# Performance work log

Hardware: AMD Instinct MI355X
Metric: run time of the kernel (lower is better)

The kernel has to match this reference:

```python
import jax, jax.numpy as jnp
import numpy as np

N = 10000      # total_num (hardcoded in GraphLearning)
BS = 100       # batch_size for per-chunk BatchNorm in training mode
C = 128        # out_channels (feature dim)
K = 50         # topk
NHID = 256     # ngcn_layers
NCLASS = 10
GAMMA = 0.01   # gamma_reg
EPS = 1e-5     # BatchNorm eps


def setup_inputs() -> dict:
    key = jax.random.key(0)
    ks = jax.random.split(key, 6)
    return {
        "inputs": jax.random.normal(ks[0], (N, 3, 32, 32), jnp.float32),
        "W_lin": jax.random.normal(ks[1], (3 * 32 * 32, C), jnp.float32) * 0.02,
        "b_lin": jnp.zeros((C,), jnp.float32),
        "bn_gamma": jnp.ones((C,), jnp.float32),
        "bn_beta": jnp.zeros((C,), jnp.float32),
        "a_S": jax.random.normal(ks[2], (C,), jnp.float32) * 0.1,
        "b_S": jnp.zeros((1,), jnp.float32),
        "W1": jax.random.normal(ks[3], (C, NHID), jnp.float32) * 0.05,
        "b1": jnp.zeros((NHID,), jnp.float32),
        "W2": jax.random.normal(ks[4], (NHID, NCLASS), jnp.float32) * 0.05,
        "b2": jnp.zeros((NCLASS,), jnp.float32),
    }


def reference(inputs, W_lin, b_lin, bn_gamma, bn_beta, a_S, b_S, W1, b1, W2, b2):
    # --- GraphLearning.forward: chunked linear + per-chunk BatchNorm (training mode) ---
    flat = inputs.reshape(N, -1)                      # [N, 3072]
    out = flat @ W_lin + b_lin                        # [N, C]
    ch = out.reshape(N // BS, BS, C)                  # per-100-row chunks, each BN'd with its own stats
    mu = ch.mean(axis=1, keepdims=True)
    var = ch.var(axis=1, keepdims=True)               # biased var, as torch BN uses
    feat = (((ch - mu) * jax.lax.rsqrt(var + EPS)).reshape(N, C)) * bn_gamma + bn_beta

    # --- construct_graph_S_loop, vectorized ---
    # per-row score: relu(a^T (x_i - x_j)^2 + b) = relu(p_i + p_j - 2 x_i diag(a) x_j^T + b)
    p = (feat ** 2) @ a_S                             # [N]
    G = (feat * a_S) @ feat.T                         # [N, N]
    scores = jax.nn.relu(p[:, None] + p[None, :] - 2.0 * G + b_S[0])
    vals, idx = jax.lax.top_k(scores, K)              # [N, K]
    soft = jax.nn.softmax(vals, axis=-1)              # softmax over each row's top-k scores
    S = jnp.zeros((N, N), feat.dtype).at[jnp.arange(N)[:, None], idx].set(soft)

    # --- loss_GL = sum(pairwise_dist * S) + gamma * sum(S); S nonzero only at (i, idx[i]) ---
    xn = (feat ** 2).sum(axis=1)                      # [N]
    nb = feat[idx]                                    # [N, K, C]
    dp = jnp.clip(xn[:, None] + xn[idx] - 2.0 * jnp.einsum('nc,nkc->nk', feat, nb), 0.0)
    loss_GL = (dp * soft).sum() + GAMMA * soft.sum()

    # --- GCN (eval mode: dropout off) ---
    h = jax.nn.relu(S @ (feat @ W1) + b1)             # gc1 + relu
    logits = S @ (h @ W2) + b2                        # gc2
    semi = jax.nn.log_softmax(logits, axis=1)
    return semi, loss_GL, S
```

## Files before the change

### kernel.cpp

```cpp
#include <hip/hip_runtime.h>
#include <hip/hip_bf16.h>
#include <cstdint>
#include <cstddef>

#define N_TOT 10000
#define CDIM  128
#define TK    50
#define NHID_ 256
#define NCLS  10
#define GAMMA_REG 0.01f
#define BN_EPS 1e-5f

typedef float f32x4 __attribute__((ext_vector_type(4)));
typedef short s16x8 __attribute__((ext_vector_type(8)));

__device__ __forceinline__ float waveSumF(float v){
  #pragma unroll
  for (int o=32;o;o>>=1) v += __shfl_xor(v,o,64);
  return v;
}
__device__ __forceinline__ float waveMaxF(float v){
  #pragma unroll
  for (int o=32;o;o>>=1) v = fmaxf(v,__shfl_xor(v,o,64));
  return v;
}
__device__ __forceinline__ int waveSumI(int v){
  #pragma unroll
  for (int o=32;o;o>>=1) v += __shfl_xor(v,o,64);
  return v;
}
__device__ __forceinline__ ushort bfh(float f){
  __hip_bfloat16 h = __float2bfloat16(f);
  return *reinterpret_cast<ushort*>(&h);
}
__device__ __forceinline__ float bf2f(ushort u){
  __hip_bfloat16 h = *reinterpret_cast<__hip_bfloat16*>(&u);
  return __bfloat162float(h);
}
__device__ __forceinline__ void gload16(const void* g, void* l){
  __builtin_amdgcn_global_load_lds(
      (const __attribute__((address_space(1))) void*)g,
      (__attribute__((address_space(3))) void*)l, 16, 0, 0);
}

template<bool BIAS>
__global__ __launch_bounds__(256) void gemm64(const float* __restrict__ A,
                                              const float* __restrict__ B,
                                              const float* __restrict__ bias,
                                              float* __restrict__ C,
                                              int M, int N, int K){
  constexpr int BK=32;
  __shared__ float As[BK][64+4];
  __shared__ float Bs[BK][64+4];
  const int tid = threadIdx.x;
  const int bm = blockIdx.y*64, bn = blockIdx.x*64;
  const int tm = (tid>>4)<<2;
  const int tn = (tid&15)<<2;
  float acc[4][4] = {};
  for (int k0=0;k0<K;k0+=BK){
    #pragma unroll
    for (int i=0;i<2;++i){
      int fi = tid + i*256;
      int r  = fi>>3;
      int c4 = fi&7;
      float4 v = make_float4(0,0,0,0);
      int gr = bm + r;
      if (gr < M) v = *(const float4*)(A + (size_t)gr*K + k0 + (c4<<2));
      As[(c4<<2)+0][r]=v.x; As[(c4<<2)+1][r]=v.y; As[(c4<<2)+2][r]=v.z; As[(c4<<2)+3][r]=v.w;
    }
    #pragma unroll
    for (int i=0;i<2;++i){
      int fi = tid + i*256;
      int r  = fi>>4;
      int c4 = fi&15;
      float4 v = *(const float4*)(B + (size_t)(k0+r)*N + bn + (c4<<2));
      *(float4*)&Bs[r][c4<<2] = v;
    }
    __syncthreads();
    #pragma unroll
    for (int kk=0;kk<BK;++kk){
      float a[4], b[4];
      *(float4*)a = *(const float4*)&As[kk][tm];
      *(float4*)b = *(const float4*)&Bs[kk][tn];
      #pragma unroll
      for (int i=0;i<4;++i)
        #pragma unroll
        for (int j=0;j<4;++j) acc[i][j] = fmaf(a[i], b[j], acc[i][j]);
    }
    __syncthreads();
  }
  #pragma unroll
  for (int i=0;i<4;++i){
    int gr = bm+tm+i;
    if (gr < M){
      float4 o; o.x=acc[i][0]; o.y=acc[i][1]; o.z=acc[i][2]; o.w=acc[i][3];
      if (BIAS){
        o.x += bias[bn+tn+0]; o.y += bias[bn+tn+1];
        o.z += bias[bn+tn+2]; o.w += bias[bn+tn+3];
      }
      *(float4*)(C + (size_t)gr*N + bn + tn) = o;
    }
  }
}

__global__ __launch_bounds__(256) void wtprep(const float* __restrict__ W,
                                              ushort* __restrict__ Wth,
                                              ushort* __restrict__ Wtl){
  __shared__ float t[64][129];
  const int tid = threadIdx.x;
  const int kb = blockIdx.x*64;
  #pragma unroll
  for (int it=0; it<8; ++it){
    int cs = it*256 + tid;
    int kr = cs >> 5;
    int c4 = cs & 31;
    float4 v = *(const float4*)(W + (size_t)(kb+kr)*128 + c4*4);
    t[kr][c4*4+0]=v.x; t[kr][c4*4+1]=v.y; t[kr][c4*4+2]=v.z; t[kr][c4*4+3]=v.w;
  }
  __syncthreads();
  #pragma unroll
  for (int it=0; it<4; ++it){
    int ch = it*256 + tid;
    int n  = ch >> 3;
    int k8 = (ch & 7)*8;
    s16x8 hv, lv;
    #pragma unroll
    for (int e=0;e<8;++e){
      float v = t[k8+e][n];
      ushort h = bfh(v);
      hv[e] = (short)h;
      lv[e] = (short)bfh(v - bf2f(h));
    }
    *(s16x8*)(Wth + (size_t)n*3072 + kb + k8) = hv;
    *(s16x8*)(Wtl + (size_t)n*3072 + kb + k8) = lv;
  }
}

__global__ __launch_bounds__(256,2) void lin_mfma(const float* __restrict__ Ain,
                                                  const ushort* __restrict__ Wth,
                                                  const ushort* __restrict__ Wtl,
                                                  float* __restrict__ P){
  extern __shared__ char lds[];
  ushort* ldsu = (ushort*)lds;
  const int tid = threadIdx.x, lane = tid&63, wave = tid>>6;
  const int wm = wave>>1, wn = wave&1;
  const int mt = blockIdx.x % 79, kc = blockIdx.x / 79;
  const int bm = mt*128;
  const int lr = lane&15, kq = lane>>4;
  f32x4 acc[4][4] = {};

  for (int st=0; st<6; ++st){
    const int kb = kc*384 + st*64;
    if (st) __syncthreads();
    #pragma unroll
    for (int it=0; it<8; ++it){
      int cs = it*256+tid, row = cs>>4, c4 = cs&15;
      int rg = bm+row; rg = rg < N_TOT ? rg : N_TOT-1;
      float4 v = *(const float4*)(Ain + (size_t)rg*3072 + kb + c4*4);
      ushort4 h, l;
      h.x=bfh(v.x); l.x=bfh(v.x-bf2f(h.x));
      h.y=bfh(v.y); l.y=bfh(v.y-bf2f(h.y));
      h.z=bfh(v.z); l.z=bfh(v.z-bf2f(h.z));
      h.w=bfh(v.w); l.w=bfh(v.w-bf2f(h.w));
      int bo = (c4*8) ^ ((row&7)<<4);
      *(ushort4*)(lds + row*128 + bo)         = h;
      *(ushort4*)(lds + 16384 + row*128 + bo) = l;
    }
    #pragma unroll
    for (int it=0; it<4; ++it){
      int cs = it*256+tid, row = cs>>3, slot = cs&7;
      int srcb = (slot*16) ^ ((row&7)<<4);
      gload16(Wth + (size_t)row*3072 + kb + (srcb>>1), ldsu + 16384 + cs*8);
      gload16(Wtl + (size_t)row*3072 + kb + (srcb>>1), ldsu + 24576 + cs*8);
    }
    __syncthreads();
    #pragma unroll
    for (int ks=0; ks<2; ++ks){
      const int kbyte = ks*64 + kq*16;
      s16x8 yh[4], yl[4];
      #pragma unroll
      for (int j=0;j<4;++j){
        int ma = wm*64 + j*16 + lr;
        int oa = ma*128 + (kbyte ^ ((ma&7)<<4));
        yh[j] = *(const s16x8*)(lds + oa);
        yl[j] = *(const s16x8*)(lds + 16384 + oa);
      }
      #pragma unroll
      for (int i=0;i<4;++i){
        int na = wn*64 + i*16 + lr;
        int ob = na*128 + (kbyte ^ ((na&7)<<4));
        s16x8 xh = *(const s16x8*)(lds + 32768 + ob);
        s16x8 xl = *(const s16x8*)(lds + 49152 + ob);
        #pragma unroll
        for (int j=0;j<4;++j){
          acc[i][j] = __builtin_amdgcn_mfma_f32_16x16x32_bf16(xh, yh[j], acc[i][j],0,0,0);
          acc[i][j] = __builtin_amdgcn_mfma_f32_16x16x32_bf16(xh, yl[j], acc[i][j],0,0,0);
          acc[i][j] = __builtin_amdgcn_mfma_f32_16x16x32_bf16(xl, yh[j], acc[i][j],0,0,0);
        }
      }
    }
  }
  #pragma unroll
  for (int j=0;j<4;++j){
    int m = bm + wm*64 + j*16 + lr;
    if (m < N_TOT){
      float* Pr = P + ((size_t)kc*N_TOT + m)*CDIM;
      #pragma unroll
      for (int i=0;i<4;++i)
        *(f32x4*)(Pr + wn*64 + i*16 + kq*4) = acc[i][j];
    }
  }
}

__global__ __launch_bounds__(256) void lin_reduce(const float* __restrict__ P,
                                                  const float* __restrict__ bias,
                                                  float* __restrict__ feat){
  int e = blockIdx.x*256 + threadIdx.x;
  float s = bias[e & 127];
  #pragma unroll
  for (int kc=0;kc<8;++kc) s += P[(size_t)kc*1280000 + e];
  feat[e] = s;
}

__global__ __launch_bounds__(512) void bn_kernel(float* __restrict__ feat,
                                                 const float* __restrict__ g,
                                                 const float* __restrict__ b){
  int chunk = blockIdx.x;
  int c = threadIdx.x & 127, rq = threadIdx.x >> 7;
  __shared__ float S1[4][128], S2[4][128];
  float* base = feat + (size_t)chunk*100*CDIM;
  float s=0.f, s2=0.f;
  for (int r=rq*25; r<rq*25+25; ++r){ float v = base[r*CDIM+c]; s+=v; s2+=v*v; }
  S1[rq][c]=s; S2[rq][c]=s2;
  __syncthreads();
  if (rq==0){
    float ts = S1[0][c]+S1[1][c]+S1[2][c]+S1[3][c];
    float t2 = S2[0][c]+S2[1][c]+S2[2][c]+S2[3][c];
    float mu = ts*0.01f;
    float var = t2*0.01f - mu*mu;
    float sc = g[c]*rsqrtf(var+BN_EPS);
    S1[0][c] = sc; S2[0][c] = b[c] - mu*sc;
  }
  __syncthreads();
  float sc = S1[0][c], sh = S2[0][c];
  for (int r=rq*25; r<rq*25+25; ++r) base[r*CDIM+c] = base[r*CDIM+c]*sc + sh;
}

__global__ __launch_bounds__(256) void featsplit(const float* __restrict__ feat,
                                                 const float* __restrict__ aS,
                                                 ushort* __restrict__ fh, ushort* __restrict__ fl,
                                                 ushort* __restrict__ gh, ushort* __restrict__ gl,
                                                 float* __restrict__ p, float* __restrict__ xn){
  int wave = threadIdx.x>>6, lane = threadIdx.x&63;
  int row = blockIdx.x*4 + wave;
  const float2 f = ((const float2*)(feat + (size_t)row*CDIM))[lane];
  const float2 a = ((const float2*)aS)[lane];
  float gx = f.x*a.x, gy = f.y*a.y;

  ushort2 v;
  size_t o = (size_t)row*64 + lane;
  v.x = bfh(f.x); v.y = bfh(f.y);
  ((ushort2*)fh)[o] = v;
  ushort2 vl; vl.x = bfh(f.x - bf2f(v.x)); vl.y = bfh(f.y - bf2f(v.y));
  ((ushort2*)fl)[o] = vl;
  ushort2 w; w.x = bfh(gx); w.y = bfh(gy);
  ((ushort2*)gh)[o] = w;
  ushort2 wl2; wl2.x = bfh(gx - bf2f(w.x)); wl2.y = bfh(gy - bf2f(w.y));
  ((ushort2*)gl)[o] = wl2;

  float sp = gx*f.x + gy*f.y;
  float sx = f.x*f.x + f.y*f.y;
  sp = waveSumF(sp); sx = waveSumF(sx);
  if (lane==0){ p[row]=sp; xn[row]=sx; }
}

__global__ __launch_bounds__(256,2) void score_mfma(const ushort* __restrict__ fh,
                                                    const ushort* __restrict__ fl,
                                                    const ushort* __restrict__ gh,
                                                    const ushort* __restrict__ gl,
                                                    const float* __restrict__ p,
                                                    const float* __restrict__ bS,
                                                    float* __restrict__ scores){
  extern __shared__ char lds[];
  ushort* ldsu = (ushort*)lds;
  const int tid  = threadIdx.x;
  const int lane = tid & 63;
  const int wave = tid >> 6;
  const int wm = wave >> 1, wn = wave & 1;

  const int nwg = 6241, q = nwg >> 3, r = nwg & 7;
  int bid = blockIdx.x;
  int xcd = bid & 7, loc = bid >> 3;
  int wid = (xcd < r ? xcd*(q+1) : r*(q+1) + (xcd-r)*q) + loc;
  const int bxt = wid / 79;
  const int byt = wid % 79;
  const int bm = byt*128;
  const int bn = bxt*128;
  const int lr = lane & 15;
  const int kq = lane >> 4;
  f32x4 acc[4][4] = {};

  for (int ko=0; ko<2; ++ko){
    const int k0 = ko*64;
    if (ko) __syncthreads();
    #define STG(SRC, RB, UOFF)                                                  \
      { _Pragma("unroll")                                                       \
        for (int it=0; it<4; ++it){                                             \
          int cs = it*256 + tid;                                                \
          int row = cs >> 3;                                                    \
          int srcb = ((cs & 7) << 4) ^ ((row & 7) << 4);                        \
          int rg = (RB) + row; rg = (rg < N_TOT ? rg : N_TOT-1);                \
          gload16(SRC + (size_t)rg*CDIM + k0 + (srcb >> 1),                     \
                  ldsu + (UOFF) + cs*8);                                        \
        } }
    STG(gh, bm, 0)
    STG(gl, bm, 8192)
    STG(fh, bn, 16384)
    STG(fl, bn, 24576)
    #undef STG
    __syncthreads();

    #pragma unroll
    for (int ks=0; ks<2; ++ks){
      const int kbyte = ks*64 + kq*16;
      s16x8 yh[4], yl[4];
      #pragma unroll
      for (int j=0;j<4;++j){
        int ca = wn*64 + j*16 + lr;
        int ob = ca*128 + (kbyte ^ ((ca&7)<<4));
        yh[j] = *(const s16x8*)(lds + 32768 + ob);
        yl[j] = *(const s16x8*)(lds + 49152 + ob);
      }
      #pragma unroll
      for (int i=0;i<4;++i){
        int ra = wm*64 + i*16 + lr;
        int oa = ra*128 + (kbyte ^ ((ra&7)<<4));
        s16x8 xh = *(const s16x8*)(lds + oa);
        s16x8 xl = *(const s16x8*)(lds + 16384 + oa);
        #pragma unroll
        for (int j=0;j<4;++j){
          acc[i][j] = __builtin_amdgcn_mfma_f32_16x16x32_bf16(xh, yh[j], acc[i][j],0,0,0);
          acc[i][j] = __builtin_amdgcn_mfma_f32_16x16x32_bf16(xh, yl[j], acc[i][j],0,0,0);
          acc[i][j] = __builtin_amdgcn_mfma_f32_16x16x32_bf16(xl, yh[j], acc[i][j],0,0,0);
        }
      }
    }
  }

  const float bb = bS[0];
  float pj[4];
  #pragma unroll
  for (int j=0;j<4;++j){
    int col = bn + wn*64 + j*16 + lr;
    pj[j] = p[col < N_TOT ? col : N_TOT-1];
  }
  #pragma unroll
  for (int i=0;i<4;++i){
    #pragma unroll
    for (int rr=0;rr<4;++rr){
      int row = bm + wm*64 + i*16 + kq*4 + rr;
      if (row < N_TOT){
        float pi = p[row];
        #pragma unroll
        for (int j=0;j<4;++j){
          int col = bn + wn*64 + j*16 + lr;
          if (col < N_TOT)
            scores[(size_t)row*N_TOT + col] = fmaxf(pi + pj[j] + bb - 2.f*acc[i][j][rr], 0.f);
        }
      }
    }
  }
}

__global__ __launch_bounds__(256) void topk_kernel(const float* __restrict__ scores,
                                                   int* __restrict__ idxO,
                                                   float* __restrict__ softO){
  const int row = blockIdx.x, tid = threadIdx.x;
  const float4* srow = (const float4*)(scores + (size_t)row*N_TOT);
  float4 v[10];
  #pragma unroll
  for (int s=0;s<10;++s){
    int fi = tid + s*256;
    v[s] = (fi < 2500) ? srow[fi] : make_float4(-1.f,-1.f,-1.f,-1.f);
  }
  float mx = -1.f;
  #pragma unroll
  for (int s=0;s<10;++s)
    mx = fmaxf(mx, fmaxf(fmaxf(v[s].x,v[s].y), fmaxf(v[s].z,v[s].w)));
  __shared__ float redf[4];
  __shared__ int cntS;
  float wm = waveMaxF(mx);
  if ((tid&63)==0) redf[tid>>6] = wm;
  __syncthreads();
  mx = fmaxf(fmaxf(redf[0],redf[1]), fmaxf(redf[2],redf[3]));

  unsigned lo = 0, hi = __float_as_uint(mx);
  while (lo < hi){
    unsigned mid = (lo + hi) >> 1;
    float t = __uint_as_float(mid);
    int c = 0;
    #pragma unroll
    for (int s=0;s<10;++s)
      c += (v[s].x>t) + (v[s].y>t) + (v[s].z>t) + (v[s].w>t);
    if (tid==0) cntS = 0;
    __syncthreads();
    c = waveSumI(c);
    if ((tid&63)==0) atomicAdd(&cntS, c);
    __syncthreads();
    int total = cntS;
    __syncthreads();
    if (total >= TK) lo = mid + 1; else hi = mid;
  }
  const float v50 = __uint_as_float(lo);

  __shared__ int   selIdx[TK];
  __shared__ float selVal[TK];
  __shared__ int cSel, cTie;
  if (tid==0){ cSel=0; cTie=0; }
  __syncthreads();
  #pragma unroll
  for (int s=0;s<10;++s){
    int base = 4*(tid + s*256);
    float vals[4] = {v[s].x, v[s].y, v[s].z, v[s].w};
    #pragma unroll
    for (int e=0;e<4;++e){
      if (vals[e] > v50){ int q = atomicAdd(&cSel,1); selIdx[q]=base+e; selVal[q]=vals[e]; }
    }
  }
  __syncthreads();
  const int m = cSel;
  #pragma unroll
  for (int s=0;s<10;++s){
    int base = 4*(tid + s*256);
    float vals[4] = {v[s].x, v[s].y, v[s].z, v[s].w};
    #pragma unroll
    for (int e=0;e<4;++e){
      if (vals[e] == v50){
        int q = atomicAdd(&cTie,1);
        if (m + q < TK){ selIdx[m+q]=base+e; selVal[m+q]=v50; }
      }
    }
  }
  __syncthreads();
  if (tid < 64){
    float e = (tid < TK) ? __expf(selVal[tid] - mx) : 0.f;
    float s = waveSumF(e);
    if (tid < TK){
      softO[row*TK + tid] = e / s;
      idxO [row*TK + tid] = selIdx[tid];
    }
  }
}

__global__ void scatter_kernel(const int* __restrict__ idx, const float* __restrict__ soft,
                               float* __restrict__ S){
  int t = blockIdx.x*blockDim.x + threadIdx.x;
  if (t < N_TOT*TK){
    int i = t / TK;
    S[(size_t)i*N_TOT + idx[t]] = soft[t];
  }
}

__global__ __launch_bounds__(256) void loss_kernel(const float* __restrict__ feat,
                                                   const float* __restrict__ xn,
                                                   const int* __restrict__ idx,
                                                   const float* __restrict__ soft,
                                                   float* __restrict__ slots){
  int row = blockIdx.x;
  int grp = threadIdx.x>>6, lane = threadIdx.x&63;
  const float2 a = ((const float2*)(feat + (size_t)row*CDIM))[lane];
  float acc = 0.f;
  for (int k=grp; k<TK; k+=4){
    int   j = idx [row*TK + k];
    float s = soft[row*TK + k];
    const float2 b = ((const float2*)(feat + (size_t)j*CDIM))[lane];
    float d = a.x*b.x + a.y*b.y;
    d = waveSumF(d);
    if (lane==0){
      float dp = fmaxf(xn[row] + xn[j] - 2.f*d, 0.f);
      acc += s*dp + GAMMA_REG*s;
    }
  }
  __shared__ float part[4];
  if (lane==0) part[grp] = acc;
  __syncthreads();
  if (threadIdx.x==0) atomicAdd(&slots[row & 255], part[0]+part[1]+part[2]+part[3]);
}

__global__ void loss_finish(const float* __restrict__ slots, float* __restrict__ lossOut){
  float v = slots[threadIdx.x];
  v = waveSumF(v);
  __shared__ float pp[4];
  if ((threadIdx.x&63)==0) pp[threadIdx.x>>6] = v;
  __syncthreads();
  if (threadIdx.x==0) lossOut[0] = pp[0]+pp[1]+pp[2]+pp[3];
}

__global__ __launch_bounds__(256) void h_kernel(const float* __restrict__ X1,
                                                const int* __restrict__ idx,
                                                const float* __restrict__ soft,
                                                const float* __restrict__ b1,
                                                float* __restrict__ h){
  int row = blockIdx.x, c = threadIdx.x;
  __shared__ int   ji[TK];
  __shared__ float sv[TK];
  if (c < TK){ ji[c]=idx[row*TK+c]; sv[c]=soft[row*TK+c]; }
  __syncthreads();
  float acc = b1[c];
  #pragma unroll 10
  for (int k=0;k<TK;++k) acc = fmaf(sv[k], X1[(size_t)ji[k]*NHID_ + c], acc);
  h[(size_t)row*NHID_ + c] = fmaxf(acc, 0.f);
}

__global__ __launch_bounds__(256) void x2_kernel(const float* __restrict__ h,
                                                 const float* __restrict__ W2,
                                                 float* __restrict__ X2){
  __shared__ float w[NHID_*NCLS];
  for (int i=threadIdx.x; i<NHID_*NCLS; i+=256) w[i] = W2[i];
  __syncthreads();
  int t = blockIdx.x*256 + threadIdx.x;
  if (t < N_TOT*NCLS){
    int r = t / NCLS, c = t % NCLS;
    float acc = 0.f;
    const float* hr = h + (size_t)r*NHID_;
    #pragma unroll 8
    for (int k=0;k<NHID_;++k) acc = fmaf(hr[k], w[k*NCLS+c], acc);
    X2[t] = acc;
  }
}

__global__ __launch_bounds__(64) void logits_kernel(const float* __restrict__ X2,
                                                    const int* __restrict__ idx,
                                                    const float* __restrict__ soft,
                                                    const float* __restrict__ b2,
                                                    float* __restrict__ semi){
  int row = blockIdx.x, tid = threadIdx.x;
  __shared__ int   ji[TK];
  __shared__ float sv[TK];
  if (tid < TK){ ji[tid]=idx[row*TK+tid]; sv[tid]=soft[row*TK+tid]; }
  __syncthreads();
  float acc = 0.f;
  if (tid < NCLS){
    acc = b2[tid];
    for (int k=0;k<TK;++k) acc = fmaf(sv[k], X2[(size_t)ji[k]*NCLS + tid], acc);
  }
  float mv = (tid < NCLS) ? acc : -1e30f;
  #pragma unroll
  for (int o=8;o;o>>=1) mv = fmaxf(mv, __shfl_xor(mv,o,16));
  float e = (tid < NCLS) ? __expf(acc - mv) : 0.f;
  #pragma unroll
  for (int o=8;o;o>>=1) e += __shfl_xor(e,o,16);
  if (tid < NCLS) semi[row*NCLS + tid] = acc - mv - logf(e);
}

extern "C" void kernel_launch(void* const* d_in, const int* in_sizes, int n_in,
                              void* d_out, int out_size, void* d_ws, size_t ws_size,
                              hipStream_t stream){
  const float* inputs   = (const float*)d_in[0];
  const float* W_lin    = (const float*)d_in[1];
  const float* b_lin    = (const float*)d_in[2];
  const float* bn_gamma = (const float*)d_in[3];
  const float* bn_beta  = (const float*)d_in[4];
  const float* a_S      = (const float*)d_in[5];
  const float* b_S      = (const float*)d_in[6];
  const float* W1       = (const float*)d_in[7];
  const float* b1       = (const float*)d_in[8];
  const float* W2       = (const float*)d_in[9];
  const float* b2       = (const float*)d_in[10];

  float* out  = (float*)d_out;
  float* ws   = (float*)d_ws;

  float*  feat = ws;
  float*  p    = ws + 1280000;
  float*  xn   = ws + 1290000;
  int*    idxb = (int*)(ws + 1300000);
  float*  soft = ws + 1800000;
  float*  X1   = ws + 2300000;
  ushort* fh   = (ushort*)(ws + 4860000);
  ushort* fl   = (ushort*)(ws + 5500000);
  ushort* gh   = (ushort*)(ws + 6140000);
  ushort* gl   = (ushort*)(ws + 6780000);
  float*  hbuf = ws + 4860000;
  float*  X2   = ws + 7420000;
  float*  lossSlots = ws + 7520000;

  float* semi    = out;
  float* lossOut = out + 100000;
  float* Sout    = out + 100001;
  float* scratch = out + 100000;

  const size_t SC = 100004;
  ushort* Wth  = (ushort*)(out + SC);
  ushort* Wtl  = (ushort*)(out + SC + 196608);
  float*  Part = out + SC + 393216;

  wtprep<<<48, 256, 0, stream>>>(W_lin, Wth, Wtl);
  lin_mfma<<<632, 256, 65536, stream>>>(inputs, Wth, Wtl, Part);
  lin_reduce<<<5000, 256, 0, stream>>>(Part, b_lin, feat);
  bn_kernel<<<100, 512, 0, stream>>>(feat, bn_gamma, bn_beta);
  featsplit<<<2500, 256, 0, stream>>>(feat, a_S, fh, fl, gh, gl, p, xn);
  score_mfma<<<6241, 256, 65536, stream>>>(fh, fl, gh, gl, p, b_S, scratch);
  gemm64<false><<<dim3(4,157), 256, 0, stream>>>(feat, W1, nullptr, X1, N_TOT, NHID_, CDIM);
  topk_kernel<<<N_TOT, 256, 0, stream>>>(scratch, idxb, soft);
  hipMemsetAsync(lossOut, 0, (size_t)100000001*sizeof(float), stream);
  hipMemsetAsync(lossSlots, 0, 256*sizeof(float), stream);
  scatter_kernel<<<(N_TOT*TK+255)/256, 256, 0, stream>>>(idxb, soft, Sout);
  loss_kernel<<<N_TOT, 256, 0, stream>>>(feat, xn, idxb, soft, lossSlots);
  loss_finish<<<1, 256, 0, stream>>>(lossSlots, lossOut);
  h_kernel<<<N_TOT, NHID_, 0, stream>>>(X1, idxb, soft, b1, hbuf);
  x2_kernel<<<(N_TOT*NCLS+255)/256, 256, 0, stream>>>(hbuf, W2, X2);
  logits_kernel<<<N_TOT, 64, 0, stream>>>(X2, idxb, soft, b2, semi);
}
```

Before: 1.156 ms.

## Compute scores in-place in S output and fuse zeroing and scatter into top-k

Score matrix is written directly into the S output buffer. The top-k kernel loads its row, zeroes it, then writes the softmax values at the selected indices. This removes the full-matrix memset and the separate scatter kernel, avoiding an extra write pass over the 400MB S. Loads become scalar because the output offset breaks 16-byte alignment.

```diff
diff --git a/kernel.cpp b/kernel.cpp
--- a/kernel.cpp
+++ b/kernel.cpp
@@ -372,16 +372,20 @@
   }
 }
 
-__global__ __launch_bounds__(256) void topk_kernel(const float* __restrict__ scores,
+__global__ __launch_bounds__(256) void topk_kernel(float* __restrict__ SrowsBase,
                                                    int* __restrict__ idxO,
                                                    float* __restrict__ softO){
   const int row = blockIdx.x, tid = threadIdx.x;
-  const float4* srow = (const float4*)(scores + (size_t)row*N_TOT);
+  float* srowW = SrowsBase + (size_t)row*N_TOT;
+  const float4* srow = (const float4*)srowW;
   float4 v[10];
   #pragma unroll
   for (int s=0;s<10;++s){
     int fi = tid + s*256;
-    v[s] = (fi < 2500) ? srow[fi] : make_float4(-1.f,-1.f,-1.f,-1.f);
+    if (fi < 2500){
+      const float* pr = srowW + fi*4;
+      v[s].x = pr[0]; v[s].y = pr[1]; v[s].z = pr[2]; v[s].w = pr[3];
+    } else v[s] = make_float4(-1.f,-1.f,-1.f,-1.f);
   }
   float mx = -1.f;
   #pragma unroll
@@ -415,6 +419,7 @@
 
   __shared__ int   selIdx[TK];
   __shared__ float selVal[TK];
+  __shared__ float softS[TK];
   __shared__ int cSel, cTie;
   if (tid==0){ cSel=0; cTie=0; }
   __syncthreads();
@@ -446,19 +451,25 @@
     float e = (tid < TK) ? __expf(selVal[tid] - mx) : 0.f;
     float s = waveSumF(e);
     if (tid < TK){
-      softO[row*TK + tid] = e / s;
+      float sv = e / s;
+      softO[row*TK + tid] = sv;
       idxO [row*TK + tid] = selIdx[tid];
-    }
-  }
-}
-
-__global__ void scatter_kernel(const int* __restrict__ idx, const float* __restrict__ soft,
-                               float* __restrict__ S){
-  int t = blockIdx.x*blockDim.x + threadIdx.x;
-  if (t < N_TOT*TK){
-    int i = t / TK;
-    S[(size_t)i*N_TOT + idx[t]] = soft[t];
-  }
+      softS[tid] = sv;
+    }
+  }
+  if (tid < 3) srowW[tid] = 0.f;
+  {
+    float4* s4 = (float4*)(srowW + 3);
+    const float4 z = make_float4(0,0,0,0);
+    #pragma unroll
+    for (int it=0; it<10; ++it){
+      int i = tid + it*256;
+      if (i < 2499) s4[i] = z;
+    }
+  }
+  if (tid == 0) srowW[9999] = 0.f;
+  __syncthreads();
+  if (tid < TK) srowW[selIdx[tid]] = softS[tid];
 }
 
 __global__ __launch_bounds__(256) void loss_kernel(const float* __restrict__ feat,
@@ -588,7 +599,6 @@
   float* semi    = out;
   float* lossOut = out + 100000;
   float* Sout    = out + 100001;
-  float* scratch = out + 100000;
 
   const size_t SC = 100004;
   ushort* Wth  = (ushort*)(out + SC);
@@ -600,12 +610,10 @@
   lin_reduce<<<5000, 256, 0, stream>>>(Part, b_lin, feat);
   bn_kernel<<<100, 512, 0, stream>>>(feat, bn_gamma, bn_beta);
   featsplit<<<2500, 256, 0, stream>>>(feat, a_S, fh, fl, gh, gl, p, xn);
-  score_mfma<<<6241, 256, 65536, stream>>>(fh, fl, gh, gl, p, b_S, scratch);
+  score_mfma<<<6241, 256, 65536, stream>>>(fh, fl, gh, gl, p, b_S, Sout);
   gemm64<false><<<dim3(4,157), 256, 0, stream>>>(feat, W1, nullptr, X1, N_TOT, NHID_, CDIM);
-  topk_kernel<<<N_TOT, 256, 0, stream>>>(scratch, idxb, soft);
-  hipMemsetAsync(lossOut, 0, (size_t)100000001*sizeof(float), stream);
+  topk_kernel<<<N_TOT, 256, 0, stream>>>(Sout, idxb, soft);
   hipMemsetAsync(lossSlots, 0, 256*sizeof(float), stream);
-  scatter_kernel<<<(N_TOT*TK+255)/256, 256, 0, stream>>>(idxb, soft, Sout);
   loss_kernel<<<N_TOT, 256, 0, stream>>>(feat, xn, idxb, soft, lossSlots);
   loss_finish<<<1, 256, 0, stream>>>(lossSlots, lossOut);
   h_kernel<<<N_TOT, NHID_, 0, stream>>>(X1, idxb, soft, b1, hbuf);
```

New measurement: 1.096 ms. 5.2% less time.
